# Performance work log

Hardware: AMD Instinct MI355X
Metric: run time of the kernel (lower is better)

The kernel has to match this reference:

```python
import jax, jax.numpy as jnp
import numpy as np

_FP8_DTYPE = jnp.float8_e4m3fn
_FP8_MAX = 448.0  # finfo(float8_e4m3fn).max


def setup_inputs() -> dict:
    key = jax.random.key(0)
    k_x, k_w = jax.random.split(key)
    B, S, IN, OUT = 2, 8192, 2048, 2048
    x = jax.random.normal(k_x, (B, S, IN), dtype=jnp.float32)
    # weight stored in fp8_e4m3fn, per-tensor scalar weight_scale
    w_f32 = jax.random.normal(k_w, (OUT, IN), dtype=jnp.float32) * 0.02
    weight = w_f32.astype(_FP8_DTYPE)
    weight_scale = jnp.asarray(1.5, dtype=jnp.float32)
    input_scale = jnp.asarray(0.75, dtype=jnp.bfloat16)  # bf16 buffer as in torch
    return {"x": x, "weight": weight, "weight_scale": weight_scale, "input_scale": input_scale}


def reference(x, weight, weight_scale, input_scale):
    orig_dtype = x.dtype
    # dequantize fp8 weight: w = fp8 * scale (in original dtype)
    w = weight.astype(orig_dtype) * weight_scale.astype(orig_dtype)
    # static fake-quant of activations: scale -> clamp -> fp8 cast -> dequant
    s_f32 = input_scale.astype(jnp.float32)
    x_scaled = x.astype(jnp.float32) / s_f32
    x_fp8 = jnp.clip(x_scaled, -_FP8_MAX, _FP8_MAX).astype(_FP8_DTYPE)
    x_qdq = x_fp8.astype(orig_dtype) * s_f32.astype(orig_dtype)
    # dense linear: [B,S,IN] @ [OUT,IN]^T -> [B,S,OUT]
    return jnp.einsum("bsi,oi->bso", x_qdq, w)
```

## Files before the change

### kernel.cpp

```cpp
#include <hip/hip_runtime.h>
#include <hip/hip_bf16.h>
#include <stdint.h>

#define M_DIM 16384
#define N_DIM 2048
#define K_DIM 2048

typedef float    f32x4 __attribute__((ext_vector_type(4)));
typedef uint32_t u32x4 __attribute__((ext_vector_type(4)));
typedef int      i32x8 __attribute__((ext_vector_type(8)));

#define SCALE_ONE 0x7F7F7F7F

__device__ inline uint32_t quant4(float4 v, float rs) {
    float q0 = fminf(fmaxf(v.x * rs, -448.f), 448.f);
    float q1 = fminf(fmaxf(v.y * rs, -448.f), 448.f);
    float q2 = fminf(fmaxf(v.z * rs, -448.f), 448.f);
    float q3 = fminf(fmaxf(v.w * rs, -448.f), 448.f);
    int p = __builtin_amdgcn_cvt_pk_fp8_f32(q0, q1, 0, false);
    p     = __builtin_amdgcn_cvt_pk_fp8_f32(q2, q3, p, true);
    return (uint32_t)p;
}

__global__ __launch_bounds__(256) void quant_xw_kernel(
    const float* __restrict__ x, const float* __restrict__ w,
    const float* __restrict__ s_ptr,
    uint32_t* __restrict__ xq, uint32_t* __restrict__ wq)
{
    if (blockIdx.x < 2048) {
        const float rs = 1.0f / s_ptr[0];
        const float4* xf4 = (const float4*)x;
        const int base = blockIdx.x * 4096 + threadIdx.x;
#pragma unroll
        for (int k = 0; k < 16; ++k) {
            const int i = base + k * 256;
            xq[i] = quant4(xf4[i], rs);
        }
    } else {
        const float4* wf4 = (const float4*)w;
        const int base = (blockIdx.x - 2048) * 1024 + threadIdx.x;
#pragma unroll
        for (int k = 0; k < 4; ++k) {
            const int i = base + k * 256;
            wq[i] = quant4(wf4[i], 1.0f);
        }
    }
}

#define G_BM 256
#define G_BN 256
#define G_NT 16
#define G_GM (M_DIM / G_BM)
#define G_GN (N_DIM / G_BN)
#define SLOT 65536

extern __shared__ uint8_t smem[];

#define MFMA_PAIR(M0, M1, A0_, A1_)                                           \
    _Pragma("unroll")                                                         \
    for (int n = 0; n < 4; ++n)                                               \
        acc[M0][n] = __builtin_amdgcn_mfma_scale_f32_16x16x128_f8f6f4(        \
            A0_, bv[n], acc[M0][n], 0, 0, 0, SCALE_ONE, 0, SCALE_ONE);        \
    _Pragma("unroll")                                                         \
    for (int n = 0; n < 4; ++n)                                               \
        acc[M1][n] = __builtin_amdgcn_mfma_scale_f32_16x16x128_f8f6f4(        \
            A1_, bv[n], acc[M1][n], 0, 0, 0, SCALE_ONE, 0, SCALE_ONE);

__global__ __launch_bounds__(512, 1) void gemm_mx_8ph(
    const uint8_t* __restrict__ Aq,
    const uint8_t* __restrict__ Wq,
    const float* __restrict__ wscale,
    const float* __restrict__ iscale,
    float* __restrict__ out)
{
    const int tid  = threadIdx.x;
    const int lane = tid & 63;
    const int wid  = tid >> 6;

    const int bid = blockIdx.x;
    const int wg  = (bid & 7) * (G_GM * G_GN / 8) + (bid >> 3);
    const int bm  = wg >> 3;
    const int bn  = wg & 7;
    const int rowBase = bm * G_BM;
    const int colBase = bn * G_BN;

    const int wrow = (wid >> 2) * 128;
    const int wcol = (wid & 3) * 64;

    const float scv = wscale[0] * iscale[0];
    asm volatile("" :: "v"(scv));

    const int sposx = (((lane & 7) ^ (lane >> 3)) * 16);
    const uint8_t* gA0 = Aq + (size_t)(rowBase + (tid >> 3)) * K_DIM + sposx;
    const uint8_t* gB0 = Wq + (size_t)(colBase + (tid >> 3)) * K_DIM + sposx;
    const int ldsW = wid * 1024;

    auto stage = [&](int buf, int tt) {
        const size_t koff = (size_t)tt * 128;
        uint8_t* sb = smem + buf * SLOT;
#pragma unroll
        for (int i = 0; i < 4; ++i)
            __builtin_amdgcn_global_load_lds(
                (const __attribute__((address_space(1))) void*)(gA0 + (size_t)i * (64 * K_DIM) + koff),
                (__attribute__((address_space(3))) void*)(sb + i * 8192 + ldsW),
                16, 0, 0);
#pragma unroll
        for (int i = 0; i < 4; ++i)
            __builtin_amdgcn_global_load_lds(
                (const __attribute__((address_space(1))) void*)(gB0 + (size_t)i * (64 * K_DIM) + koff),
                (__attribute__((address_space(3))) void*)(sb + 32768 + i * 8192 + ldsW),
                16, 0, 0);
    };

    const int fr  = lane & 15;
    const int pLo = (((lane >> 4) * 2) ^ (fr & 7)) * 16;

    auto readA = [&](const uint8_t* sb, int m) -> i32x8 {
        const int ro = (wrow + m * 16 + fr) * 128;
        u32x4 lo = *(const u32x4*)(sb + ro + pLo);
        u32x4 hi = *(const u32x4*)(sb + ro + (pLo ^ 16));
        return (i32x8){(int)lo.x, (int)lo.y, (int)lo.z, (int)lo.w,
                       (int)hi.x, (int)hi.y, (int)hi.z, (int)hi.w};
    };
    auto readB = [&](const uint8_t* sb, int n) -> i32x8 {
        const int ro = 32768 + (wcol + n * 16 + fr) * 128;
        u32x4 lo = *(const u32x4*)(sb + ro + pLo);
        u32x4 hi = *(const u32x4*)(sb + ro + (pLo ^ 16));
        return (i32x8){(int)lo.x, (int)lo.y, (int)lo.z, (int)lo.w,
                       (int)hi.x, (int)hi.y, (int)hi.z, (int)hi.w};
    };

    f32x4 acc[8][4] = {};

    stage(0, 0);
    asm volatile("s_waitcnt vmcnt(0)" ::: "memory");
    __builtin_amdgcn_s_barrier();
    __builtin_amdgcn_sched_barrier(0);

    for (int t = 0; t < G_NT; ++t) {
        const int cur = t & 1;
        const uint8_t* sb = smem + cur * SLOT;

        i32x8 bv[4];
#pragma unroll
        for (int n = 0; n < 4; ++n) bv[n] = readB(sb, n);
        i32x8 aE0 = readA(sb, 0), aE1 = readA(sb, 1);
        if (t + 1 < G_NT) stage(cur ^ 1, t + 1);
        __builtin_amdgcn_sched_barrier(0);
        __builtin_amdgcn_s_barrier();
        asm volatile("s_waitcnt lgkmcnt(0)" ::: "memory");
        __builtin_amdgcn_sched_barrier(0);
        __builtin_amdgcn_s_setprio(1);
        MFMA_PAIR(0, 1, aE0, aE1)
        __builtin_amdgcn_s_setprio(0);
        __builtin_amdgcn_sched_barrier(0);
        __builtin_amdgcn_s_barrier();

        i32x8 aO0 = readA(sb, 2), aO1 = readA(sb, 3);
        __builtin_amdgcn_sched_barrier(0);
        __builtin_amdgcn_s_barrier();
        asm volatile("s_waitcnt lgkmcnt(0)" ::: "memory");
        __builtin_amdgcn_sched_barrier(0);
        __builtin_amdgcn_s_setprio(1);
        MFMA_PAIR(2, 3, aO0, aO1)
        __builtin_amdgcn_s_setprio(0);
        __builtin_amdgcn_sched_barrier(0);
        __builtin_amdgcn_s_barrier();

        aE0 = readA(sb, 4); aE1 = readA(sb, 5);
        __builtin_amdgcn_sched_barrier(0);
        __builtin_amdgcn_s_barrier();
        asm volatile("s_waitcnt lgkmcnt(0)" ::: "memory");
        __builtin_amdgcn_sched_barrier(0);
        __builtin_amdgcn_s_setprio(1);
        MFMA_PAIR(4, 5, aE0, aE1)
        __builtin_amdgcn_s_setprio(0);
        __builtin_amdgcn_sched_barrier(0);
        __builtin_amdgcn_s_barrier();

        aO0 = readA(sb, 6); aO1 = readA(sb, 7);
        __builtin_amdgcn_sched_barrier(0);
        __builtin_amdgcn_s_barrier();
        asm volatile("s_waitcnt lgkmcnt(0)" ::: "memory");
        __builtin_amdgcn_sched_barrier(0);
        __builtin_amdgcn_s_setprio(1);
        MFMA_PAIR(6, 7, aO0, aO1)
        __builtin_amdgcn_s_setprio(0);
        __builtin_amdgcn_sched_barrier(0);
        asm volatile("s_waitcnt vmcnt(0)" ::: "memory");
        __builtin_amdgcn_s_barrier();
        __builtin_amdgcn_sched_barrier(0);
    }

    const int crow = (lane >> 4) << 2;
    const int ccol = lane & 15;
#pragma unroll
    for (int m = 0; m < 8; ++m) {
#pragma unroll
        for (int n = 0; n < 4; ++n) {
            const size_t base = (size_t)(rowBase + wrow + m * 16 + crow) * N_DIM
                              + (colBase + wcol + n * 16 + ccol);
#pragma unroll
            for (int r = 0; r < 4; ++r)
                out[base + (size_t)r * N_DIM] = acc[m][n][r] * scv;
        }
    }
}

__global__ __launch_bounds__(256) void fused_fp8_gemm(
    const float* __restrict__ X, const float* __restrict__ Wf,
    const float* __restrict__ wscale, const float* __restrict__ iscale,
    float* __restrict__ out)
{
    __shared__ uint8_t smA[2][128 * 64];
    __shared__ uint8_t smB[2][128 * 64];

    const int tid  = threadIdx.x;
    const int lane = tid & 63;
    const int wid  = tid >> 6;

    const float s  = iscale[0];
    const float rs = 1.0f / s;
    const float sc = wscale[0] * s;

    const int bid = blockIdx.x;
    const int wg  = (bid & 7) * 256 + (bid >> 3);
    const int bm  = wg >> 4;
    const int bn  = wg & 15;
    const int rowBase = bm * 128;
    const int colBase = bn * 128;
    const int wrow = (wid >> 1) * 64;
    const int wcol = (wid & 1) * 64;
    const int ar = tid >> 1;
    const int ah = (tid & 1) * 32;

    const float* Xrow = X  + (size_t)(rowBase + ar) * K_DIM;
    const float* Wrow = Wf + (size_t)(colBase + ar) * K_DIM;

    float4 areg[8], breg[8];
    auto load_tile = [&](int kt) {
        const int k0 = kt * 64;
#pragma unroll
        for (int j = 0; j < 8; ++j) areg[j] = *(const float4*)(Xrow + k0 + ah + j * 4);
#pragma unroll
        for (int j = 0; j < 8; ++j) breg[j] = *(const float4*)(Wrow + k0 + ah + j * 4);
    };
    auto write_tile = [&](int buf) {
        uint32_t aq[8], bq[8];
#pragma unroll
        for (int j = 0; j < 8; ++j) { aq[j] = quant4(areg[j], rs); bq[j] = quant4(breg[j], 1.0f); }
        *(u32x4*)&smA[buf][ar * 64 + ah]      = *(const u32x4*)&aq[0];
        *(u32x4*)&smA[buf][ar * 64 + ah + 16] = *(const u32x4*)&aq[4];
        *(u32x4*)&smB[buf][ar * 64 + ah]      = *(const u32x4*)&bq[0];
        *(u32x4*)&smB[buf][ar * 64 + ah + 16] = *(const u32x4*)&bq[4];
    };

    f32x4 acc[4][4] = {};
    load_tile(0); write_tile(0); __syncthreads();
    for (int kt = 0; kt < 32; ++kt) {
        const int cur = kt & 1;
        if (kt + 1 < 32) load_tile(kt + 1);
        const uint8_t* pA = smA[cur];
        const uint8_t* pB = smB[cur];
        const int afr = lane & 15, koff = (lane >> 4) << 3;
#pragma unroll
        for (int kk = 0; kk < 2; ++kk) {
            long long a[4], b[4];
#pragma unroll
            for (int m = 0; m < 4; ++m)
                a[m] = *(const long long*)(pA + (wrow + m * 16 + afr) * 64 + kk * 32 + koff);
#pragma unroll
            for (int n = 0; n < 4; ++n)
                b[n] = *(const long long*)(pB + (wcol + n * 16 + afr) * 64 + kk * 32 + koff);
#pragma unroll
            for (int m = 0; m < 4; ++m)
#pragma unroll
                for (int n = 0; n < 4; ++n)
                    acc[m][n] = __builtin_amdgcn_mfma_f32_16x16x32_fp8_fp8(
                        a[m], b[n], acc[m][n], 0, 0, 0);
        }
        if (kt + 1 < 32) write_tile(cur ^ 1);
        __syncthreads();
    }
    const int crow = (lane >> 4) << 2, ccol = lane & 15;
#pragma unroll
    for (int m = 0; m < 4; ++m)
#pragma unroll
        for (int n = 0; n < 4; ++n) {
            const size_t base = (size_t)(rowBase + wrow + m * 16 + crow) * N_DIM
                              + (colBase + wcol + n * 16 + ccol);
#pragma unroll
            for (int r = 0; r < 4; ++r)
                out[base + (size_t)r * N_DIM] = acc[m][n][r] * sc;
        }
}

extern "C" void kernel_launch(void* const* d_in, const int* in_sizes, int n_in,
                              void* d_out, int out_size, void* d_ws, size_t ws_size,
                              hipStream_t stream) {
    const float* x      = (const float*)d_in[0];
    const float* w      = (const float*)d_in[1];
    const float* wscale = (const float*)d_in[2];
    const float* iscale = (const float*)d_in[3];
    float*       out    = (float*)d_out;

    const size_t needA = (size_t)M_DIM * K_DIM;
    const size_t needW = (size_t)N_DIM * K_DIM;

    hipError_t e = hipFuncSetAttribute((const void*)gemm_mx_8ph,
                                       hipFuncAttributeMaxDynamicSharedMemorySize,
                                       2 * SLOT);

    if (e == hipSuccess && ws_size >= needA + needW) {
        uint32_t* xq = (uint32_t*)d_ws;
        uint32_t* wq = (uint32_t*)((uint8_t*)d_ws + needA);
        quant_xw_kernel<<<3072, 256, 0, stream>>>(x, w, iscale, xq, wq);
        gemm_mx_8ph<<<G_GM * G_GN, 512, 2 * SLOT, stream>>>(
            (const uint8_t*)xq, (const uint8_t*)wq, wscale, iscale, out);
    } else {
        fused_fp8_gemm<<<2048, 256, 0, stream>>>(x, w, wscale, iscale, out);
    }
}
```

Baseline: 119.4 us.

## Restructure GEMM main loop into two phases with split prefetch staging

Replaces the four-phase K-loop body, where each phase read two A fragments and issued 8 MFMAs, with two phases that each read four A fragments and issue 16 MFMAs. The global-to-LDS prefetch of the next K tile is now split across the two phases. This removes two barrier/waitcnt rounds per iteration and gives longer MFMA bursts. In exchange it holds more A fragments live in registers, and the launch-bounds min-blocks hint is dropped, which may change register allocation.

```diff
diff --git a/kernel.cpp b/kernel.cpp
--- a/kernel.cpp
+++ b/kernel.cpp
@@ -56,17 +56,7 @@
 
 extern __shared__ uint8_t smem[];
 
-#define MFMA_PAIR(M0, M1, A0_, A1_)                                           \
-    _Pragma("unroll")                                                         \
-    for (int n = 0; n < 4; ++n)                                               \
-        acc[M0][n] = __builtin_amdgcn_mfma_scale_f32_16x16x128_f8f6f4(        \
-            A0_, bv[n], acc[M0][n], 0, 0, 0, SCALE_ONE, 0, SCALE_ONE);        \
-    _Pragma("unroll")                                                         \
-    for (int n = 0; n < 4; ++n)                                               \
-        acc[M1][n] = __builtin_amdgcn_mfma_scale_f32_16x16x128_f8f6f4(        \
-            A1_, bv[n], acc[M1][n], 0, 0, 0, SCALE_ONE, 0, SCALE_ONE);
-
-__global__ __launch_bounds__(512, 1) void gemm_mx_8ph(
+__global__ __launch_bounds__(512) void gemm_mx_2ph(
     const uint8_t* __restrict__ Aq,
     const uint8_t* __restrict__ Wq,
     const float* __restrict__ wscale,
@@ -95,21 +85,20 @@
     const uint8_t* gB0 = Wq + (size_t)(colBase + (tid >> 3)) * K_DIM + sposx;
     const int ldsW = wid * 1024;
 
-    auto stage = [&](int buf, int tt) {
+    auto stageHalf = [&](int buf, int tt, int h) {
         const size_t koff = (size_t)tt * 128;
         uint8_t* sb = smem + buf * SLOT;
 #pragma unroll
-        for (int i = 0; i < 4; ++i)
+        for (int i = 2 * h; i < 2 * h + 2; ++i) {
             __builtin_amdgcn_global_load_lds(
                 (const __attribute__((address_space(1))) void*)(gA0 + (size_t)i * (64 * K_DIM) + koff),
                 (__attribute__((address_space(3))) void*)(sb + i * 8192 + ldsW),
                 16, 0, 0);
-#pragma unroll
-        for (int i = 0; i < 4; ++i)
             __builtin_amdgcn_global_load_lds(
                 (const __attribute__((address_space(1))) void*)(gB0 + (size_t)i * (64 * K_DIM) + koff),
                 (__attribute__((address_space(3))) void*)(sb + 32768 + i * 8192 + ldsW),
                 16, 0, 0);
+        }
     };
 
     const int fr  = lane & 15;
@@ -132,7 +121,7 @@
 
     f32x4 acc[8][4] = {};
 
-    stage(0, 0);
+    stageHalf(0, 0, 0); stageHalf(0, 0, 1);
     asm volatile("s_waitcnt vmcnt(0)" ::: "memory");
     __builtin_amdgcn_s_barrier();
     __builtin_amdgcn_sched_barrier(0);
@@ -141,50 +130,40 @@
         const int cur = t & 1;
         const uint8_t* sb = smem + cur * SLOT;
 
-        i32x8 bv[4];
+        i32x8 bv[4], av[4];
 #pragma unroll
         for (int n = 0; n < 4; ++n) bv[n] = readB(sb, n);
-        i32x8 aE0 = readA(sb, 0), aE1 = readA(sb, 1);
-        if (t + 1 < G_NT) stage(cur ^ 1, t + 1);
+#pragma unroll
+        for (int m = 0; m < 4; ++m) av[m] = readA(sb, m);
+        if (t + 1 < G_NT) stageHalf(cur ^ 1, t + 1, 0);
         __builtin_amdgcn_sched_barrier(0);
         __builtin_amdgcn_s_barrier();
         asm volatile("s_waitcnt lgkmcnt(0)" ::: "memory");
         __builtin_amdgcn_sched_barrier(0);
         __builtin_amdgcn_s_setprio(1);
-        MFMA_PAIR(0, 1, aE0, aE1)
+#pragma unroll
+        for (int m = 0; m < 4; ++m)
+#pragma unroll
+            for (int n = 0; n < 4; ++n)
+                acc[m][n] = __builtin_amdgcn_mfma_scale_f32_16x16x128_f8f6f4(
+                    av[m], bv[n], acc[m][n], 0, 0, 0, SCALE_ONE, 0, SCALE_ONE);
         __builtin_amdgcn_s_setprio(0);
         __builtin_amdgcn_sched_barrier(0);
-        __builtin_amdgcn_s_barrier();
-
-        i32x8 aO0 = readA(sb, 2), aO1 = readA(sb, 3);
+
+#pragma unroll
+        for (int m = 0; m < 4; ++m) av[m] = readA(sb, m + 4);
+        if (t + 1 < G_NT) stageHalf(cur ^ 1, t + 1, 1);
         __builtin_amdgcn_sched_barrier(0);
         __builtin_amdgcn_s_barrier();
         asm volatile("s_waitcnt lgkmcnt(0)" ::: "memory");
         __builtin_amdgcn_sched_barrier(0);
         __builtin_amdgcn_s_setprio(1);
-        MFMA_PAIR(2, 3, aO0, aO1)
-        __builtin_amdgcn_s_setprio(0);
-        __builtin_amdgcn_sched_barrier(0);
-        __builtin_amdgcn_s_barrier();
-
-        aE0 = readA(sb, 4); aE1 = readA(sb, 5);
-        __builtin_amdgcn_sched_barrier(0);
-        __builtin_amdgcn_s_barrier();
-        asm volatile("s_waitcnt lgkmcnt(0)" ::: "memory");
-        __builtin_amdgcn_sched_barrier(0);
-        __builtin_amdgcn_s_setprio(1);
-        MFMA_PAIR(4, 5, aE0, aE1)
-        __builtin_amdgcn_s_setprio(0);
-        __builtin_amdgcn_sched_barrier(0);
-        __builtin_amdgcn_s_barrier();
-
-        aO0 = readA(sb, 6); aO1 = readA(sb, 7);
-        __builtin_amdgcn_sched_barrier(0);
-        __builtin_amdgcn_s_barrier();
-        asm volatile("s_waitcnt lgkmcnt(0)" ::: "memory");
-        __builtin_amdgcn_sched_barrier(0);
-        __builtin_amdgcn_s_setprio(1);
-        MFMA_PAIR(6, 7, aO0, aO1)
+#pragma unroll
+        for (int m = 0; m < 4; ++m)
+#pragma unroll
+            for (int n = 0; n < 4; ++n)
+                acc[m + 4][n] = __builtin_amdgcn_mfma_scale_f32_16x16x128_f8f6f4(
+                    av[m], bv[n], acc[m + 4][n], 0, 0, 0, SCALE_ONE, 0, SCALE_ONE);
         __builtin_amdgcn_s_setprio(0);
         __builtin_amdgcn_sched_barrier(0);
         asm volatile("s_waitcnt vmcnt(0)" ::: "memory");
@@ -307,7 +286,7 @@
     const size_t needA = (size_t)M_DIM * K_DIM;
     const size_t needW = (size_t)N_DIM * K_DIM;
 
-    hipError_t e = hipFuncSetAttribute((const void*)gemm_mx_8ph,
+    hipError_t e = hipFuncSetAttribute((const void*)gemm_mx_2ph,
                                        hipFuncAttributeMaxDynamicSharedMemorySize,
                                        2 * SLOT);
 
@@ -315,7 +294,7 @@
         uint32_t* xq = (uint32_t*)d_ws;
         uint32_t* wq = (uint32_t*)((uint8_t*)d_ws + needA);
         quant_xw_kernel<<<3072, 256, 0, stream>>>(x, w, iscale, xq, wq);
-        gemm_mx_8ph<<<G_GM * G_GN, 512, 2 * SLOT, stream>>>(
+        gemm_mx_2ph<<<G_GM * G_GN, 512, 2 * SLOT, stream>>>(
             (const uint8_t*)xq, (const uint8_t*)wq, wscale, iscale, out);
     } else {
         fused_fp8_gemm<<<2048, 256, 0, stream>>>(x, w, wscale, iscale, out);
```

New measurement: 115.6 us. 3.2% less time.
